# Performance work log

Measured on AMD Instinct MI355X. Metric: run time of the kernel, lower is better.

The kernel has to match this reference:

```python
import jax, jax.numpy as jnp
import numpy as np

D_MODEL = 1024
H = 16
D_V = 64
B = 4
N = 1024
LARGE_NEG = -1000000000.0


def setup_inputs() -> dict:
    key = jax.random.key(0)
    k_x, k_q, k_k, k_v, k_o = jax.random.split(key, 5)
    X = jax.random.normal(k_x, (B, N, D_MODEL), dtype=jnp.float32)
    W_q = jax.random.normal(k_q, (H, D_MODEL, D_MODEL), dtype=jnp.float32)
    W_k = jax.random.normal(k_k, (H, D_MODEL, D_MODEL), dtype=jnp.float32)
    W_v = jax.random.normal(k_v, (H, D_MODEL, D_V), dtype=jnp.float32)
    W_o = jax.random.normal(k_o, (H * D_V, D_MODEL), dtype=jnp.float32)
    return {"X": X, "W_q": W_q, "W_k": W_k, "W_v": W_v, "W_o": W_o}


def reference(X, W_q, W_k, W_v, W_o):
    Bb, Nn, Dd = X.shape
    scale = 1.0 / jnp.sqrt(jnp.asarray(Dd, dtype=X.dtype))
    # Per-head projections, batched over heads instead of a Python loop.
    Q = jnp.einsum('bnd,hde->bhne', X, W_q)          # [B,H,N,d_model]
    K = jnp.einsum('bnd,hde->bhne', X, W_k)          # [B,H,N,d_model]
    V = jnp.einsum('bnd,hdv->bhnv', X, W_v)          # [B,H,N,D_v]
    scores = jnp.einsum('bhne,bhme->bhnm', Q, K) * scale  # [B,H,N,N]
    A = jax.nn.softmax(scores, axis=-1)
    Hh = jnp.einsum('bhnm,bhmv->bhnv', A, V)         # [B,H,N,D_v]
    concat = Hh.transpose(0, 2, 1, 3).reshape(Bb, Nn, -1)  # [B,N,H*D_v]
    Y = concat @ W_o                                  # [B,N,d_model]
    # Post-hoc mask: triu over the LAST TWO dims (N, d_model), diagonal=1.
    mask = jnp.triu(jnp.ones((Nn, Dd), dtype=bool), k=1)
    return jnp.where(mask[None, :, :], jnp.asarray(LARGE_NEG, Y.dtype), Y)
```

## Files before the change

### kernel.cpp

```cpp
#include <hip/hip_runtime.h>
#include <stdint.h>

typedef short s16x8 __attribute__((ext_vector_type(8)));
typedef float f32x4 __attribute__((ext_vector_type(4)));

__device__ __forceinline__ unsigned short f2bf(float f) {
  union { float f; unsigned int u; } v; v.f = f;
  unsigned int r = v.u + 0x7FFFu + ((v.u >> 16) & 1u);
  return (unsigned short)(r >> 16);
}

__device__ __forceinline__ unsigned cvt2fp8(float a, float b) {
#if __has_builtin(__builtin_amdgcn_cvt_pk_fp8_f32)
  return (unsigned)__builtin_amdgcn_cvt_pk_fp8_f32(a, b, 0, false);
#else
  unsigned r;
  asm("v_cvt_pk_fp8_f32 %0, %1, %2" : "=v"(r) : "v"(a), "v"(b));
  return r;
#endif
}

__device__ __forceinline__ void gload_lds16(const void* g, void* l) {
  __builtin_amdgcn_global_load_lds(
      (const __attribute__((address_space(1))) unsigned int*)g,
      (__attribute__((address_space(3))) unsigned int*)l, 16, 0, 0);
}

__device__ __forceinline__ unsigned xcd_swz(unsigned fid, unsigned nwg) {
  unsigned cpx = nwg >> 3;
  return (fid & 7) * cpx + (fid >> 3);
}

__global__ void conv_fp8(const float* __restrict__ in, unsigned char* __restrict__ out, int n8) {
  int i = blockIdx.x * blockDim.x + threadIdx.x;
  if (i >= n8) return;
  const f32x4* p = (const f32x4*)(in + (long)i * 8);
  f32x4 a = p[0], b = p[1];
  unsigned long w = (unsigned long)(cvt2fp8(a[0], a[1]) & 0xFFFFu)
                  | ((unsigned long)(cvt2fp8(a[2], a[3]) & 0xFFFFu) << 16)
                  | ((unsigned long)(cvt2fp8(b[0], b[1]) & 0xFFFFu) << 32)
                  | ((unsigned long)(cvt2fp8(b[2], b[3]) & 0xFFFFu) << 48);
  *(unsigned long*)(out + (long)i * 8) = w;
}

__global__ void convT_wv_f8(const float* __restrict__ in, unsigned char* __restrict__ out) {
  int i = blockIdx.x * blockDim.x + threadIdx.x;
  int v = i & 63, d = (i >> 6) & 1023, h = i >> 16;
  out[((long)h * 64 + v) * 1024 + d] = (unsigned char)cvt2fp8(in[i], 0.f);
}

__global__ void convT_wo(const float* __restrict__ in, unsigned short* __restrict__ out) {
  int i = blockIdx.x * blockDim.x + threadIdx.x;
  int e = i & 1023, c = i >> 10;
  out[(long)e * 1024 + c] = f2bf(in[i]);
}

template<int BM, int BN, int WAVES_M, int WAVES_N, int CMODE>
__global__ __launch_bounds__(256, 2)
void gemm_bt(const unsigned short* __restrict__ A, const unsigned short* __restrict__ BT,
             void* __restrict__ Cout, int aDiv, long aStr, int bMod, long bStr,
             long cStr, int ldc)
{
  constexpr int BK = 64;
  constexpr int FM = BM / (WAVES_M * 16);
  constexpr int FN = BN / (WAVES_N * 16);
  __shared__ __align__(16) unsigned short At[BM * BK];
  __shared__ __align__(16) unsigned short Bt[BN * BK];

  unsigned fid = blockIdx.x + gridDim.x * (blockIdx.y + gridDim.y * blockIdx.z);
  unsigned nwg = gridDim.x * gridDim.y * gridDim.z;
  unsigned sid = xcd_swz(fid, nwg);
  unsigned bx = sid % gridDim.x;
  unsigned rem = sid / gridDim.x;
  unsigned by = rem % gridDim.y;
  unsigned bz = rem / gridDim.y;

  const int t = threadIdx.x;
  const int l = t & 63;
  const int g = l >> 4, c = l & 15;
  const int w = t >> 6;
  const int wr = (w / WAVES_N) * (BM / WAVES_M);
  const int wc = (w % WAVES_N) * (BN / WAVES_N);
  const int z = bz;
  const int m0 = by * BM;
  const int n0 = bx * BN;
  const unsigned short* Ab = A + (long)(z / aDiv) * aStr + (long)m0 * 1024;
  const unsigned short* Bb = BT + (long)(z % bMod) * bStr + (long)n0 * 1024;

  const long cbase = (long)z * cStr;

  if constexpr (CMODE == 2) {
    if (n0 > m0 + BM - 1) {
#pragma unroll
      for (int m = 0; m < FM; ++m)
#pragma unroll
        for (int n = 0; n < FN; ++n)
#pragma unroll
          for (int r = 0; r < 4; ++r) {
            int row = wr + m * 16 + g * 4 + r;
            int col = n0 + wc + n * 16 + c;
            ((float*)Cout)[cbase + (long)(m0 + row) * ldc + col] = -1e9f;
          }
      return;
    }
  }

  f32x4 acc[FM][FN] = {};
  constexpr int PA = (BM * BK) / 2048;
  constexpr int PB = (BN * BK) / 2048;

  for (int k0 = 0; k0 < 1024; k0 += BK) {
#pragma unroll
    for (int p = 0; p < PA; ++p) {
      int e = (p * 256 + t) * 8;
      int row = e >> 6, col = e & 63;
      gload_lds16(Ab + (long)row * 1024 + k0 + col, &At[e]);
    }
#pragma unroll
    for (int p = 0; p < PB; ++p) {
      int e = (p * 256 + t) * 8;
      int row = e >> 6, col = e & 63;
      gload_lds16(Bb + (long)row * 1024 + k0 + col, &Bt[e]);
    }
    __syncthreads();
#pragma unroll
    for (int kk = 0; kk < BK; kk += 32) {
      s16x8 af[FM], bf[FN];
#pragma unroll
      for (int m = 0; m < FM; ++m)
        af[m] = *(const s16x8*)&At[(wr + m * 16 + c) * BK + kk + g * 8];
#pragma unroll
      for (int n = 0; n < FN; ++n)
        bf[n] = *(const s16x8*)&Bt[(wc + n * 16 + c) * BK + kk + g * 8];
#pragma unroll
      for (int m = 0; m < FM; ++m)
#pragma unroll
        for (int n = 0; n < FN; ++n)
          acc[m][n] = __builtin_amdgcn_mfma_f32_16x16x32_bf16(af[m], bf[n], acc[m][n], 0, 0, 0);
    }
    __syncthreads();
  }

#pragma unroll
  for (int m = 0; m < FM; ++m)
#pragma unroll
    for (int n = 0; n < FN; ++n)
#pragma unroll
      for (int r = 0; r < 4; ++r) {
        int row = wr + m * 16 + g * 4 + r;
        int col = n0 + wc + n * 16 + c;
        int grow = m0 + row;
        float v = acc[m][n][r];
        if constexpr (CMODE == 0) {
          ((unsigned short*)Cout)[cbase + (long)grow * ldc + col] = f2bf(v);
        } else if constexpr (CMODE == 2) {
          ((float*)Cout)[cbase + (long)grow * ldc + col] = (col > grow) ? -1e9f : v;
        }
      }
}

template<int BM, int BN, int WM, int WN, int TRANS>
__global__ __launch_bounds__(256, 2)
void gemm_f8(const unsigned char* __restrict__ A, const unsigned char* __restrict__ BT,
             unsigned char* __restrict__ Cout, int aDiv, long aStr, int bMod, long bStr,
             long cStr, int ldc, float scale)
{
  constexpr int FM = BM / (WM * 16);
  constexpr int FN = BN / (WN * 16);
  __shared__ __align__(16) unsigned char At[BM * 128];
  __shared__ __align__(16) unsigned char Bt[BN * 128];

  unsigned fid = blockIdx.x + gridDim.x * (blockIdx.y + gridDim.y * blockIdx.z);
  unsigned nwg = gridDim.x * gridDim.y * gridDim.z;
  unsigned sid = xcd_swz(fid, nwg);
  unsigned bx = sid % gridDim.x;
  unsigned rem = sid / gridDim.x;
  unsigned by = rem % gridDim.y;
  unsigned bz = rem / gridDim.y;

  const int t = threadIdx.x;
  const int l = t & 63;
  const int g = l >> 4, c = l & 15;
  const int w = t >> 6;
  const int wr = (w / WN) * (BM / WM);
  const int wc = (w % WN) * (BN / WN);
  const int z = bz;
  const int m0 = by * BM;
  const int n0 = bx * BN;
  const unsigned char* Ab = A + (long)(z / aDiv) * aStr + (long)m0 * 1024;
  const unsigned char* Bb = BT + (long)(z % bMod) * bStr + (long)n0 * 1024;

  f32x4 acc[FM][FN] = {};
  constexpr int PA = (BM * 128) / (256 * 16);
  constexpr int PB = (BN * 128) / (256 * 16);

  for (int k0 = 0; k0 < 1024; k0 += 128) {
#pragma unroll
    for (int p = 0; p < PA; ++p) {
      int e = (p * 256 + t) * 16;
      int r = e >> 7, u = (e >> 4) & 7;
      int gcol = ((u ^ (r & 7)) << 4);
      gload_lds16(Ab + (long)r * 1024 + k0 + gcol, &At[e]);
    }
#pragma unroll
    for (int p = 0; p < PB; ++p) {
      int e = (p * 256 + t) * 16;
      int r = e >> 7, u = (e >> 4) & 7;
      int gcol = ((u ^ (r & 7)) << 4);
      gload_lds16(Bb + (long)r * 1024 + k0 + gcol, &Bt[e]);
    }
    __syncthreads();
#pragma unroll
    for (int kk = 0; kk < 128; kk += 32) {
      long af[FM], bf[FN];
#pragma unroll
      for (int m = 0; m < FM; ++m) {
        int row = wr + m * 16 + c;
        int un = (kk >> 4) + (g >> 1);
        af[m] = *(const long*)&At[row * 128 + ((un ^ (row & 7)) << 4) + (g & 1) * 8];
      }
#pragma unroll
      for (int n = 0; n < FN; ++n) {
        int row = wc + n * 16 + c;
        int un = (kk >> 4) + (g >> 1);
        bf[n] = *(const long*)&Bt[row * 128 + ((un ^ (row & 7)) << 4) + (g & 1) * 8];
      }
      __builtin_amdgcn_s_setprio(1);
#pragma unroll
      for (int m = 0; m < FM; ++m)
#pragma unroll
        for (int n = 0; n < FN; ++n)
          acc[m][n] = __builtin_amdgcn_mfma_f32_16x16x32_fp8_fp8(af[m], bf[n], acc[m][n], 0, 0, 0);
      __builtin_amdgcn_s_setprio(0);
    }
    __syncthreads();
  }

  const long cbase = (long)z * cStr;
#pragma unroll
  for (int m = 0; m < FM; ++m)
#pragma unroll
    for (int n = 0; n < FN; ++n) {
      int row0 = m0 + wr + m * 16 + g * 4;
      int col  = n0 + wc + n * 16 + c;
      unsigned p01 = cvt2fp8(acc[m][n][0] * scale, acc[m][n][1] * scale);
      unsigned p23 = cvt2fp8(acc[m][n][2] * scale, acc[m][n][3] * scale);
      if constexpr (TRANS == 0) {
        unsigned char* Cp = Cout + cbase + (long)row0 * ldc + col;
        Cp[0]            = (unsigned char)p01;
        Cp[(long)ldc]    = (unsigned char)(p01 >> 8);
        Cp[(long)ldc*2]  = (unsigned char)p23;
        Cp[(long)ldc*3]  = (unsigned char)(p23 >> 8);
      } else {
        unsigned word = (p01 & 0xFFFFu) | (p23 << 16);
        *(unsigned*)(Cout + cbase + (long)col * ldc + row0) = word;
      }
    }
}

__global__ __launch_bounds__(256, 2)
void flash_attn(const unsigned char* __restrict__ R, const unsigned char* __restrict__ X,
                const unsigned char* __restrict__ VT, unsigned short* __restrict__ Yc)
{
  __shared__ __align__(16) unsigned char Sh[40960];
  unsigned char* Qt  = Sh;
  unsigned char* Kt  = Sh + 16384;
  unsigned char* Vt8 = Sh + 32768;
  unsigned char* Pl8 = Sh;

  unsigned fid = blockIdx.x + gridDim.x * blockIdx.y;
  unsigned nwg = gridDim.x * gridDim.y;
  unsigned sid = xcd_swz(fid, nwg);
  const int q0 = (sid % gridDim.x) * 128;
  const int bh = sid / gridDim.x;

  const int t = threadIdx.x;
  const int l = t & 63;
  const int w = t >> 6;
  const int g = l >> 4;
  const int c = l & 15;
  const int b = bh >> 4;

  const unsigned char* Qq = X + (long)b * (1024 * 1024) + (long)q0 * 1024;
  const unsigned char* Kb = R + (long)bh * (1024 * 1024);
  const unsigned char* Vb = VT + (long)bh * (64 * 1024);

  f32x4 accO[2][4] = {};
  float mrun[2][4], lrun[2][4];
#pragma unroll
  for (int m = 0; m < 2; ++m)
#pragma unroll
    for (int r = 0; r < 4; ++r) { mrun[m][r] = -1e30f; lrun[m][r] = 0.f; }

  const float scale = 8.0f;

  for (int m0 = 0; m0 < 1024; m0 += 128) {
    f32x4 accS[2][8] = {};
    for (int k0 = 0; k0 < 1024; k0 += 128) {
#pragma unroll
      for (int p = 0; p < 4; ++p) {
        int e = (p * 256 + t) * 16;
        int r = e >> 7, u = (e >> 4) & 7;
        int gcol = ((u ^ (r & 7)) << 4);
        gload_lds16(Qq + (long)r * 1024 + k0 + gcol, &Qt[e]);
      }
#pragma unroll
      for (int p = 0; p < 4; ++p) {
        int e = (p * 256 + t) * 16;
        int r = e >> 7, u = (e >> 4) & 7;
        int gcol = ((u ^ (r & 7)) << 4);
        gload_lds16(Kb + (long)(m0 + r) * 1024 + k0 + gcol, &Kt[e]);
      }
      __syncthreads();
#pragma unroll
      for (int kk = 0; kk < 128; kk += 32) {
        long af[2], bf[8];
#pragma unroll
        for (int m = 0; m < 2; ++m) {
          int row = w * 32 + m * 16 + c;
          int un = (kk >> 4) + (g >> 1);
          af[m] = *(const long*)&Qt[row * 128 + ((un ^ (row & 7)) << 4) + (g & 1) * 8];
        }
#pragma unroll
        for (int n = 0; n < 8; ++n) {
          int row = n * 16 + c;
          int un = (kk >> 4) + (g >> 1);
          bf[n] = *(const long*)&Kt[row * 128 + ((un ^ (row & 7)) << 4) + (g & 1) * 8];
        }
        __builtin_amdgcn_s_setprio(1);
#pragma unroll
        for (int m = 0; m < 2; ++m)
#pragma unroll
          for (int n = 0; n < 8; ++n)
            accS[m][n] = __builtin_amdgcn_mfma_f32_16x16x32_fp8_fp8(af[m], bf[n], accS[m][n], 0, 0, 0);
        __builtin_amdgcn_s_setprio(0);
      }
      __syncthreads();
    }
#pragma unroll
    for (int p = 0; p < 2; ++p) {
      int e = (p * 256 + t) * 16;
      int r = e >> 7, u = (e >> 4) & 7;
      int gcol = ((u ^ (r & 7)) << 4);
      gload_lds16(Vb + (long)r * 1024 + m0 + gcol, &Vt8[e]);
    }
    float alpha[2][4];
#pragma unroll
    for (int m = 0; m < 2; ++m) {
#pragma unroll
      for (int r = 0; r < 4; ++r) {
        float mx = -1e30f;
#pragma unroll
        for (int n = 0; n < 8; ++n) mx = fmaxf(mx, accS[m][n][r]);
#pragma unroll
        for (int s = 1; s < 16; s <<= 1) mx = fmaxf(mx, __shfl_xor(mx, s));
        mx *= scale;
        float mnew = fmaxf(mrun[m][r], mx);
        float a = __expf(mrun[m][r] - mnew);
        alpha[m][r] = a;
        float sum = 0.f;
#pragma unroll
        for (int n = 0; n < 8; ++n) {
          float pe = __expf(accS[m][n][r] * scale - mnew);
          accS[m][n][r] = pe;
          sum += pe;
        }
#pragma unroll
        for (int s = 1; s < 16; s <<= 1) sum += __shfl_xor(sum, s);
        lrun[m][r] = lrun[m][r] * a + sum;
        mrun[m][r] = mnew;
      }
    }
#pragma unroll
    for (int m = 0; m < 2; ++m)
#pragma unroll
      for (int n = 0; n < 8; ++n)
#pragma unroll
        for (int r = 0; r < 4; ++r) {
          int row = w * 32 + m * 16 + g * 4 + r;
          Pl8[row * 128 + ((n ^ (row & 7)) << 4) + c] =
              (unsigned char)cvt2fp8(accS[m][n][r], 0.f);
        }
    __syncthreads();
#pragma unroll
    for (int m = 0; m < 2; ++m)
#pragma unroll
      for (int n = 0; n < 4; ++n)
#pragma unroll
        for (int r = 0; r < 4; ++r)
          accO[m][n][r] *= alpha[m][r];
#pragma unroll
    for (int kk = 0; kk < 128; kk += 32) {
      long pa[2], vb[4];
#pragma unroll
      for (int m = 0; m < 2; ++m) {
        int row = w * 32 + m * 16 + c;
        int un = (kk >> 4) + (g >> 1);
        pa[m] = *(const long*)&Pl8[row * 128 + ((un ^ (row & 7)) << 4) + (g & 1) * 8];
      }
#pragma unroll
      for (int n = 0; n < 4; ++n) {
        int row = n * 16 + c;
        int un = (kk >> 4) + (g >> 1);
        vb[n] = *(const long*)&Vt8[row * 128 + ((un ^ (row & 7)) << 4) + (g & 1) * 8];
      }
      __builtin_amdgcn_s_setprio(1);
#pragma unroll
      for (int m = 0; m < 2; ++m)
#pragma unroll
        for (int n = 0; n < 4; ++n)
          accO[m][n] = __builtin_amdgcn_mfma_f32_16x16x32_fp8_fp8(pa[m], vb[n], accO[m][n], 0, 0, 0);
      __builtin_amdgcn_s_setprio(0);
    }
    __syncthreads();
  }
  unsigned short* out = Yc + (long)b * (1024 * 1024) + (long)(bh & 15) * 64;
#pragma unroll
  for (int m = 0; m < 2; ++m)
#pragma unroll
    for (int n = 0; n < 4; ++n)
#pragma unroll
      for (int r = 0; r < 4; ++r) {
        int row = q0 + w * 32 + m * 16 + g * 4 + r;
        int col = n * 16 + c;
        out[(long)row * 1024 + col] = f2bf(accO[m][n][r] / lrun[m][r]);
      }
}

extern "C" void kernel_launch(void* const* d_in, const int* in_sizes, int n_in,
                              void* d_out, int out_size, void* d_ws, size_t ws_size,
                              hipStream_t stream) {
  (void)in_sizes; (void)n_in; (void)out_size; (void)ws_size;
  const float* X  = (const float*)d_in[0];
  const float* Wq = (const float*)d_in[1];
  const float* Wk = (const float*)d_in[2];
  const float* Wv = (const float*)d_in[3];
  const float* Wo = (const float*)d_in[4];
  float* Y = (float*)d_out;
  char* ws = (char*)d_ws;

  const long MB = 1L << 20;
  unsigned char*  Xf8   = (unsigned char*)(ws + 0);
  unsigned char*  Wqf8  = (unsigned char*)(ws + 4  * MB);
  unsigned char*  Wkf8  = (unsigned char*)(ws + 20 * MB);
  unsigned char*  Mf8   = (unsigned char*)(ws + 36 * MB);
  unsigned char*  WvTf8 = (unsigned char*)(ws + 52 * MB);
  unsigned char*  VTb8  = (unsigned char*)(ws + 56 * MB);
  unsigned short* Ccat  = (unsigned short*)(ws + 60 * MB);
  unsigned short* WoT   = (unsigned short*)(ws + 68 * MB);
  unsigned char*  Rf8   = (unsigned char*)(ws + 72 * MB);

  const long M1 = 1L << 20;

  conv_fp8<<<2048, 256, 0, stream>>>(X,  Xf8,  524288);
  conv_fp8<<<8192, 256, 0, stream>>>(Wq, Wqf8, 2097152);
  conv_fp8<<<8192, 256, 0, stream>>>(Wk, Wkf8, 2097152);
  convT_wv_f8<<<4096, 256, 0, stream>>>(Wv, WvTf8);

  gemm_f8<128, 128, 2, 2, 0><<<dim3(8, 8, 16), 256, 0, stream>>>(
      Wqf8, Wkf8, Mf8, 1, M1, 16, M1, M1, 1024, 0.00390625f);

  gemm_f8<128, 128, 2, 2, 0><<<dim3(8, 8, 64), 256, 0, stream>>>(
      Xf8, Mf8, Rf8, 16, M1, 16, M1, M1, 1024, 1.0f);

  gemm_f8<128, 64, 4, 1, 1><<<dim3(1, 8, 64), 256, 0, stream>>>(
      Xf8, WvTf8, VTb8, 16, M1, 16, 65536, 65536, 1024, 1.0f);

  flash_attn<<<dim3(8, 64), 256, 0, stream>>>(Rf8, Xf8, VTb8, Ccat);

  convT_wo<<<4096, 256, 0, stream>>>(Wo, WoT);
  gemm_bt<128, 128, 2, 2, 2><<<dim3(8, 8, 4), 256, 0, stream>>>(
      Ccat, WoT, Y, 1, M1, 1, 0, M1, 1024);
}
```

Baseline: 337.4 us.

## Split flash attention over the key dimension and merge partial results

The flash attention kernel now splits the 1024 keys into two halves, doubling the grid from 512 to 1024 workgroups so the GPU's compute units are better filled. Each half writes unnormalised fp32 partial outputs plus running max and sum to workspace. A new merge kernel combines them with log-sum-exp rescaling and writes bf16. Launch bounds are raised to 4 waves per SIMD. This adds an extra kernel launch, extra global traffic for the partials, and possible register pressure from the tighter launch bound.

```diff
diff --git a/kernel.cpp b/kernel.cpp
--- a/kernel.cpp
+++ b/kernel.cpp
@@ -2,6 +2,7 @@
 #include <stdint.h>
 
 typedef short s16x8 __attribute__((ext_vector_type(8)));
+typedef short s16x4 __attribute__((ext_vector_type(4)));
 typedef float f32x4 __attribute__((ext_vector_type(4)));
 
 __device__ __forceinline__ unsigned short f2bf(float f) {
@@ -258,9 +259,10 @@
     }
 }
 
-__global__ __launch_bounds__(256, 2)
+__global__ __launch_bounds__(256, 4)
 void flash_attn(const unsigned char* __restrict__ R, const unsigned char* __restrict__ X,
-                const unsigned char* __restrict__ VT, unsigned short* __restrict__ Yc)
+                const unsigned char* __restrict__ VT,
+                float* __restrict__ Opart, float* __restrict__ ML)
 {
   __shared__ __align__(16) unsigned char Sh[40960];
   unsigned char* Qt  = Sh;
@@ -271,8 +273,10 @@
   unsigned fid = blockIdx.x + gridDim.x * blockIdx.y;
   unsigned nwg = gridDim.x * gridDim.y;
   unsigned sid = xcd_swz(fid, nwg);
-  const int q0 = (sid % gridDim.x) * 128;
-  const int bh = sid / gridDim.x;
+  const int q0    = (sid % gridDim.x) * 128;
+  const int rest  = sid / gridDim.x;
+  const int bh    = rest >> 1;
+  const int split = rest & 1;
 
   const int t = threadIdx.x;
   const int l = t & 63;
@@ -294,7 +298,8 @@
 
   const float scale = 8.0f;
 
-  for (int m0 = 0; m0 < 1024; m0 += 128) {
+  const int mlo = split * 512, mhi = mlo + 512;
+  for (int m0 = mlo; m0 < mhi; m0 += 128) {
     f32x4 accS[2][8] = {};
     for (int k0 = 0; k0 < 1024; k0 += 128) {
 #pragma unroll
@@ -414,7 +419,8 @@
     }
     __syncthreads();
   }
-  unsigned short* out = Yc + (long)b * (1024 * 1024) + (long)(bh & 15) * 64;
+  const int part = (bh << 1) + split;
+  float* Op = Opart + (long)part * 65536;
 #pragma unroll
   for (int m = 0; m < 2; ++m)
 #pragma unroll
@@ -423,8 +429,45 @@
       for (int r = 0; r < 4; ++r) {
         int row = q0 + w * 32 + m * 16 + g * 4 + r;
         int col = n * 16 + c;
-        out[(long)row * 1024 + col] = f2bf(accO[m][n][r] / lrun[m][r]);
-      }
+        Op[(long)row * 64 + col] = accO[m][n][r];
+      }
+  if (c == 0) {
+#pragma unroll
+    for (int m = 0; m < 2; ++m)
+#pragma unroll
+      for (int r = 0; r < 4; ++r) {
+        int row = q0 + w * 32 + m * 16 + g * 4 + r;
+        ML[(long)part * 2048 + row * 2]     = mrun[m][r];
+        ML[(long)part * 2048 + row * 2 + 1] = lrun[m][r];
+      }
+  }
+}
+
+__global__ void flash_merge(const float* __restrict__ Opart, const float* __restrict__ ML,
+                            unsigned short* __restrict__ Yc)
+{
+  int i = blockIdx.x * blockDim.x + threadIdx.x;
+  int bh  = i >> 14;
+  int rem = i & 16383;
+  int row = rem >> 4;
+  int v4  = (rem & 15) * 4;
+  int p0 = bh << 1;
+  float m0 = ML[(long)p0 * 2048 + row * 2];
+  float l0 = ML[(long)p0 * 2048 + row * 2 + 1];
+  float m1 = ML[(long)(p0 + 1) * 2048 + row * 2];
+  float l1 = ML[(long)(p0 + 1) * 2048 + row * 2 + 1];
+  float mn = fmaxf(m0, m1);
+  float a0 = __expf(m0 - mn), a1 = __expf(m1 - mn);
+  float inv = 1.f / (l0 * a0 + l1 * a1);
+  f32x4 o0 = *(const f32x4*)&Opart[(long)p0 * 65536 + (long)row * 64 + v4];
+  f32x4 o1 = *(const f32x4*)&Opart[(long)(p0 + 1) * 65536 + (long)row * 64 + v4];
+  int b = bh >> 4, h = bh & 15;
+  s16x4 o;
+  o[0] = (short)f2bf((o0[0] * a0 + o1[0] * a1) * inv);
+  o[1] = (short)f2bf((o0[1] * a0 + o1[1] * a1) * inv);
+  o[2] = (short)f2bf((o0[2] * a0 + o1[2] * a1) * inv);
+  o[3] = (short)f2bf((o0[3] * a0 + o1[3] * a1) * inv);
+  *(s16x4*)(Yc + (long)b * (1024 * 1024) + (long)row * 1024 + h * 64 + v4) = o;
 }
 
 extern "C" void kernel_launch(void* const* d_in, const int* in_sizes, int n_in,
@@ -449,6 +492,8 @@
   unsigned short* Ccat  = (unsigned short*)(ws + 60 * MB);
   unsigned short* WoT   = (unsigned short*)(ws + 68 * MB);
   unsigned char*  Rf8   = (unsigned char*)(ws + 72 * MB);
+  float*          Opart = (float*)(ws + 136 * MB);
+  float*          MLb   = (float*)(ws + 168 * MB);
 
   const long M1 = 1L << 20;
 
@@ -466,7 +511,8 @@
   gemm_f8<128, 64, 4, 1, 1><<<dim3(1, 8, 64), 256, 0, stream>>>(
       Xf8, WvTf8, VTb8, 16, M1, 16, 65536, 65536, 1024, 1.0f);
 
-  flash_attn<<<dim3(8, 64), 256, 0, stream>>>(Rf8, Xf8, VTb8, Ccat);
+  flash_attn<<<dim3(8, 128), 256, 0, stream>>>(Rf8, Xf8, VTb8, Opart, MLb);
+  flash_merge<<<4096, 256, 0, stream>>>(Opart, MLb, Ccat);
 
   convT_wo<<<4096, 256, 0, stream>>>(Wo, WoT);
   gemm_bt<128, 128, 2, 2, 2><<<dim3(8, 8, 4), 256, 0, stream>>>(
```

Measured after the change: 404.7 us. 20.0% more time.
